# Kernel tuning notes

Measured on AMD Instinct MI355X. Metric: run time of the kernel, lower is better.

## Reference

```python
import jax, jax.numpy as jnp
import numpy as np

NH = 8       # num attention heads (hardcoded in module)
NL = 6       # n_layers
EPS = 1e-5   # LayerNorm eps (torch default)


def pos_enc(dim, length):
    # faithful to module's positional_encoding: even cols sin, odd cols cos,
    # with angle = pos / 10000^(2i/dim) where i indexes ALL columns via arange(0,2*dim,2)/dim
    pos = jnp.arange(length, dtype=jnp.float32)[:, None]
    div = 1.0 / (10000.0 ** (jnp.arange(0, 2 * dim, 2, dtype=jnp.float32) / dim))
    ang = pos * div[None, :]  # [length, dim]
    cols = jnp.arange(dim)
    return jnp.where(cols % 2 == 0, jnp.sin(ang), jnp.cos(ang))


def layernorm(x):
    m = x.mean(-1, keepdims=True)
    v = x.var(-1, keepdims=True)  # biased, matches torch LayerNorm
    return (x - m) / jnp.sqrt(v + EPS)


def setup_inputs() -> dict:
    key = jax.random.key(0)
    ks = jax.random.split(key, 8)
    S, H = 2048, 1024
    D = H // NH
    sc = 1.0 / np.sqrt(H)  # ~ torch Linear init scale
    return {
        "inputs": jax.random.normal(ks[0], (S, H), jnp.float32),
        "Wq": jax.random.normal(ks[1], (NH, H, D), jnp.float32) * sc,
        "bq": jnp.zeros((NH, D), jnp.float32),
        "Wk": jax.random.normal(ks[2], (NH, H, D), jnp.float32) * sc,
        "bk": jnp.zeros((NH, D), jnp.float32),
        "Wv": jax.random.normal(ks[3], (NH, H, D), jnp.float32) * sc,
        "bv": jnp.zeros((NH, D), jnp.float32),
        "W1": jax.random.normal(ks[4], (H, H), jnp.float32) * sc,
        "b1": jnp.zeros((H,), jnp.float32),
        "W2": jax.random.normal(ks[5], (H, H), jnp.float32) * sc,
        "b2": jnp.zeros((H,), jnp.float32),
    }


def reference(inputs, Wq, bq, Wk, bk, Wv, bv, W1, b1, W2, b2):
    S, H = inputs.shape
    scale = jnp.sqrt(jnp.float32(H))  # module scales by sqrt(hidden), not sqrt(head_dim)
    x = inputs + pos_enc(H, S)        # [S, H]
    kv = x  # dropout in eval mode = identity; k_v_input fixed to layer-0 input (faithful)
    # K/V are identical every layer (shared weights + fixed kv input)
    K = jnp.einsum('sh,nhd->nsd', kv, Wk) + bk[:, None, :]  # [NH, S, D]
    V = jnp.einsum('sh,nhd->nsd', kv, Wv) + bv[:, None, :]
    t_in = x
    for _ in range(NL):
        Q = jnp.einsum('sh,nhd->nsd', t_in, Wq) + bq[:, None, :]
        A = jax.nn.softmax(jnp.einsum('nsd,ntd->nst', Q, K) / scale, axis=-1)
        ctx = jnp.einsum('nst,ntd->nsd', A, V)        # [NH, S, D]
        cat = ctx.transpose(1, 0, 2).reshape(S, H)    # concat heads on feature dim
        mh = layernorm(t_in + cat)
        ff = jax.nn.relu(mh @ W1 + b1) @ W2 + b2
        t_in = layernorm(mh + ff)
    return t_in
```

## Files before the change

kernel.cpp:

```cpp
#include <hip/hip_runtime.h>

#define S_LEN 2048
#define H_DIM 1024
#define NHEAD 8
#define D_HEAD 128
#define KSPLIT 4
#define KV_PER (S_LEN / KSPLIT)

typedef __bf16 bf16x8 __attribute__((ext_vector_type(8)));
typedef float floatx4 __attribute__((ext_vector_type(4)));

__device__ __forceinline__ float b2f(unsigned short u) {
    union { unsigned int i; float f; } v;
    v.i = ((unsigned int)u) << 16;
    return v.f;
}
__device__ __forceinline__ unsigned short f2b(float f) {
    union { float f; unsigned int i; } v;
    v.f = f;
    return (unsigned short)((v.i + 0x7fffu + ((v.i >> 16) & 1u)) >> 16);
}

__device__ __forceinline__ void dma16(void* lds, const void* g) {
    __builtin_amdgcn_global_load_lds(
        (const __attribute__((address_space(1))) void*)g,
        (__attribute__((address_space(3))) void*)lds, 16, 0, 0);
}

__global__ __launch_bounds__(256) void posenc_kernel(
    const float* __restrict__ in, float* __restrict__ xf,
    unsigned short* __restrict__ xb)
{
    int g = blockIdx.x * 256 + threadIdx.x;
    int s = g >> 10;
    int h = g & 1023;
    float dv = powf(10000.0f, -(float)h * (1.0f / 512.0f));
    float ang = (float)s * dv;
    float pe = (h & 1) ? cosf(ang) : sinf(ang);
    float x = in[g] + pe;
    xf[g] = x;
    xb[g] = f2b(x);
}

__global__ __launch_bounds__(256) void transpose_f2b(
    const float* __restrict__ in, unsigned short* __restrict__ out, int R, int C)
{
    __shared__ unsigned short tile[32][33];
    const float* ih = in + (size_t)blockIdx.z * R * C;
    unsigned short* oh = out + (size_t)blockIdx.z * R * C;
    int r0 = blockIdx.y * 32, c0 = blockIdx.x * 32;
    int tx = threadIdx.x, ty = threadIdx.y;
    for (int i = ty; i < 32; i += 8)
        tile[i][tx] = f2b(ih[(size_t)(r0 + i) * C + c0 + tx]);
    __syncthreads();
    for (int i = ty; i < 32; i += 8)
        oh[(size_t)(c0 + i) * R + r0 + tx] = tile[tx][i];
}

template <int MODE, bool RELU>
__global__ __launch_bounds__(256, 4) void gemm_bt(
    const unsigned short* __restrict__ A, const unsigned short* __restrict__ Bt,
    const float* __restrict__ bias, float* __restrict__ Cf,
    unsigned short* __restrict__ Cb, int M, int N, int K, int ldt)
{
    __shared__ __align__(16) unsigned short sA[2][64 * 64];
    __shared__ __align__(16) unsigned short sB[2][64 * 64];
    const int tid = threadIdx.x;
    const int wave = tid >> 6, lane = tid & 63;
    const int quad = lane >> 4, l16 = lane & 15;
    const int i0 = blockIdx.y * 64, j0 = blockIdx.x * 64;
    const int wm = (wave >> 1) * 32, wn = (wave & 1) * 32;

    const int srow = lane >> 3;
    const int schunk = (lane & 7) ^ (srow & 7);
    const unsigned short* Ap0 = A + (size_t)(i0 + wave * 8 + srow) * K + schunk * 8;
    const unsigned short* Ap1 = A + (size_t)(i0 + 32 + wave * 8 + srow) * K + schunk * 8;
    const unsigned short* Bp0 = Bt + (size_t)(j0 + wave * 8 + srow) * K + schunk * 8;
    const unsigned short* Bp1 = Bt + (size_t)(j0 + 32 + wave * 8 + srow) * K + schunk * 8;
    const int ld0 = (wave * 8) * 64, ld1 = (32 + wave * 8) * 64;

    floatx4 z4 = {0.f, 0.f, 0.f, 0.f};
    floatx4 acc[2][2];
#pragma unroll
    for (int i = 0; i < 2; i++)
#pragma unroll
        for (int j = 0; j < 2; j++) acc[i][j] = z4;

    dma16(sA[0] + ld0, Ap0);
    dma16(sA[0] + ld1, Ap1);
    dma16(sB[0] + ld0, Bp0);
    dma16(sB[0] + ld1, Bp1);
    __syncthreads();

    int buf = 0;
    for (int k0 = 0; k0 < K; k0 += 64) {
        if (k0 + 64 < K) {
            dma16(sA[buf ^ 1] + ld0, Ap0 + k0 + 64);
            dma16(sA[buf ^ 1] + ld1, Ap1 + k0 + 64);
            dma16(sB[buf ^ 1] + ld0, Bp0 + k0 + 64);
            dma16(sB[buf ^ 1] + ld1, Bp1 + k0 + 64);
        }
        const unsigned short* cA = sA[buf];
        const unsigned short* cB = sB[buf];
#pragma unroll
        for (int kh = 0; kh < 2; kh++) {
            bf16x8 af[2], bfr[2];
#pragma unroll
            for (int mi = 0; mi < 2; mi++) {
                int row = wm + mi * 16 + l16;
                int p = (kh * 4 + quad) ^ (l16 & 7);
                af[mi] = *(const bf16x8*)(cA + row * 64 + p * 8);
            }
#pragma unroll
            for (int ni = 0; ni < 2; ni++) {
                int row = wn + ni * 16 + l16;
                int p = (kh * 4 + quad) ^ (l16 & 7);
                bfr[ni] = *(const bf16x8*)(cB + row * 64 + p * 8);
            }
#pragma unroll
            for (int mi = 0; mi < 2; mi++)
#pragma unroll
                for (int ni = 0; ni < 2; ni++)
                    acc[mi][ni] = __builtin_amdgcn_mfma_f32_16x16x32_bf16(
                        af[mi], bfr[ni], acc[mi][ni], 0, 0, 0);
        }
        __syncthreads();
        buf ^= 1;
    }

#pragma unroll
    for (int mi = 0; mi < 2; mi++) {
#pragma unroll
        for (int ni = 0; ni < 2; ni++) {
            const int col = j0 + wn + ni * 16 + l16;
            const float bval = bias[col];
#pragma unroll
            for (int r = 0; r < 4; r++) {
                const int row_o = i0 + wm + mi * 16 + quad * 4 + r;
                float v = acc[mi][ni][r] + bval;
                if (RELU) v = fmaxf(v, 0.0f);
                if (MODE == 0) Cb[(size_t)row_o * N + col] = f2b(v);
                else if (MODE == 1) Cb[(size_t)col * ldt + row_o] = f2b(v);
                else Cf[(size_t)row_o * N + col] = v;
            }
        }
    }
}

__global__ __launch_bounds__(256, 3) void flash_attn(
    const unsigned short* __restrict__ Qg, const unsigned short* __restrict__ Kg,
    const unsigned short* __restrict__ Vt, unsigned short* __restrict__ Op,
    float* __restrict__ Lp)
{
    __shared__ __align__(16) unsigned short sK[64 * 128];
    __shared__ __align__(16) unsigned short sV[128 * 64];

    const int tid = threadIdx.x;
    const int wave = tid >> 6, lane = tid & 63;
    const int quad = lane >> 4, l16 = lane & 15;
    const int head = blockIdx.y;
    const int q0 = blockIdx.x * 64;
    const int split = blockIdx.z;
    const int h0 = head * D_HEAD;

    bf16x8 aq[4];
    const int qrow = q0 + wave * 16 + l16;
#pragma unroll
    for (int ks = 0; ks < 4; ks++)
        aq[ks] = *(const bf16x8*)(Qg + (size_t)qrow * H_DIM + h0 + ks * 32 + quad * 8);

    unsigned short* myP = sK + wave * (16 * 72);

    const int k_r = wave * 4 + (lane >> 4);
    const int k_c = (lane & 15) ^ (k_r & 15);
    const int v_r = wave * 8 + (lane >> 3);
    const int v_c = (lane & 7) ^ (v_r & 7);

    const unsigned short* Kbase = Kg + h0;
    const unsigned short* Vbase = Vt + (size_t)h0 * S_LEN;
    const int kt0 = split * KV_PER;

    floatx4 z4 = {0.f, 0.f, 0.f, 0.f};
    floatx4 o[8];
#pragma unroll
    for (int i = 0; i < 8; i++) o[i] = z4;
    float l_r[4] = {0.f, 0.f, 0.f, 0.f};

    for (int it0 = 0; it0 < KV_PER; it0 += 64) {
        const int t0 = kt0 + it0;
        __syncthreads();
#pragma unroll
        for (int it = 0; it < 4; it++) {
            dma16(sK + (wave * 4 + it * 16) * 128,
                  Kbase + (size_t)(t0 + k_r + it * 16) * H_DIM + k_c * 8);
            dma16(sV + (wave * 8 + it * 32) * 64,
                  Vbase + (size_t)(v_r + it * 32) * S_LEN + t0 + v_c * 8);
        }
        __syncthreads();

        floatx4 sc[4];
#pragma unroll
        for (int ni = 0; ni < 4; ni++) {
            sc[ni] = z4;
#pragma unroll
            for (int ks = 0; ks < 4; ks++) {
                int p = (ks * 4 + quad) ^ l16;
                bf16x8 bk = *(const bf16x8*)(sK + (ni * 16 + l16) * 128 + p * 8);
                sc[ni] = __builtin_amdgcn_mfma_f32_16x16x32_bf16(aq[ks], bk, sc[ni], 0, 0, 0);
            }
        }

#pragma unroll
        for (int ni = 0; ni < 4; ni++)
#pragma unroll
            for (int r = 0; r < 4; r++) {
                float p = __expf(sc[ni][r] * 0.03125f);
                sc[ni][r] = p;
                l_r[r] += p;
            }

        __syncthreads();
#pragma unroll
        for (int ni = 0; ni < 4; ni++)
#pragma unroll
            for (int r = 0; r < 4; r++) {
                int prow = quad * 4 + r;
                myP[prow * 72 + ((ni * 16 + l16) ^ ((prow & 8) << 1))] = f2b(sc[ni][r]);
            }
        bf16x8 ap[2];
#pragma unroll
        for (int ks = 0; ks < 2; ks++)
            ap[ks] = *(const bf16x8*)(myP + l16 * 72 + ((ks * 32 + quad * 8) ^ ((l16 & 8) << 1)));
#pragma unroll
        for (int ni = 0; ni < 8; ni++) {
#pragma unroll
            for (int ks = 0; ks < 2; ks++) {
                int p = (ks * 4 + quad) ^ (l16 & 7);
                bf16x8 bv = *(const bf16x8*)(sV + (ni * 16 + l16) * 64 + p * 8);
                o[ni] = __builtin_amdgcn_mfma_f32_16x16x32_bf16(ap[ks], bv, o[ni], 0, 0, 0);
            }
        }
    }

#pragma unroll
    for (int r = 0; r < 4; r++)
#pragma unroll
        for (int off = 1; off < 16; off <<= 1)
            l_r[r] += __shfl_xor(l_r[r], off, 64);

#pragma unroll
    for (int r = 0; r < 4; r++) {
        float inv = 1.0f / l_r[r];
        int row = q0 + wave * 16 + quad * 4 + r;
#pragma unroll
        for (int ni = 0; ni < 8; ni++)
            Op[((size_t)split * S_LEN + row) * H_DIM + h0 + ni * 16 + l16] =
                f2b(o[ni][r] * inv);
        if (l16 == 0)
            Lp[(split * NHEAD + head) * S_LEN + row] = l_r[r];
    }
}

__global__ __launch_bounds__(256) void merge_add_layernorm(
    const float* __restrict__ t, const unsigned short* __restrict__ Op,
    const float* __restrict__ Lp,
    float* __restrict__ of, unsigned short* __restrict__ ob)
{
    __shared__ float red[8];
    const int row = blockIdx.x, tid = threadIdx.x;
    const int head = tid >> 5;
    const size_t base = (size_t)row * H_DIM + tid * 4;

    float l_s[KSPLIT];
    ushort4 os[KSPLIT];
#pragma unroll
    for (int sp = 0; sp < KSPLIT; sp++) {
        os[sp] = *(const ushort4*)(Op + ((size_t)sp * S_LEN + row) * H_DIM + tid * 4);
        l_s[sp] = Lp[(sp * NHEAD + head) * S_LEN + row];
    }
    float W = 0.f, a0 = 0.f, a1 = 0.f, a2 = 0.f, a3 = 0.f;
#pragma unroll
    for (int sp = 0; sp < KSPLIT; sp++) {
        float w = l_s[sp];
        W += w;
        a0 += w * b2f(os[sp].x);
        a1 += w * b2f(os[sp].y);
        a2 += w * b2f(os[sp].z);
        a3 += w * b2f(os[sp].w);
    }
    float inv = 1.0f / W;
    float4 x = *(const float4*)(t + base);
    float v0 = x.x + a0 * inv, v1 = x.y + a1 * inv;
    float v2 = x.z + a2 * inv, v3 = x.w + a3 * inv;

    float s = v0 + v1 + v2 + v3;
    float q = v0 * v0 + v1 * v1 + v2 * v2 + v3 * v3;
#pragma unroll
    for (int off = 32; off >= 1; off >>= 1) {
        s += __shfl_xor(s, off, 64);
        q += __shfl_xor(q, off, 64);
    }
    if ((tid & 63) == 0) { red[tid >> 6] = s; red[4 + (tid >> 6)] = q; }
    __syncthreads();
    s = red[0] + red[1] + red[2] + red[3];
    q = red[4] + red[5] + red[6] + red[7];
    const float mean = s * (1.0f / (float)H_DIM);
    const float var = q * (1.0f / (float)H_DIM) - mean * mean;
    const float rstd = rsqrtf(var + 1e-5f);
    float o0 = (v0 - mean) * rstd, o1 = (v1 - mean) * rstd;
    float o2 = (v2 - mean) * rstd, o3 = (v3 - mean) * rstd;
    *(float4*)(of + base) = make_float4(o0, o1, o2, o3);
    *(ushort4*)(ob + base) = make_ushort4(f2b(o0), f2b(o1), f2b(o2), f2b(o3));
}

__global__ __launch_bounds__(256) void add_layernorm(
    const float* __restrict__ a, const float* __restrict__ b,
    float* __restrict__ of, unsigned short* __restrict__ ob)
{
    __shared__ float red[8];
    const int row = blockIdx.x, tid = threadIdx.x;
    const size_t base = (size_t)row * H_DIM + tid * 4;
    float4 x = *(const float4*)(a + base);
    float4 y = *(const float4*)(b + base);
    float v0 = x.x + y.x, v1 = x.y + y.y, v2 = x.z + y.z, v3 = x.w + y.w;
    float s = v0 + v1 + v2 + v3;
    float q = v0 * v0 + v1 * v1 + v2 * v2 + v3 * v3;
#pragma unroll
    for (int off = 32; off >= 1; off >>= 1) {
        s += __shfl_xor(s, off, 64);
        q += __shfl_xor(q, off, 64);
    }
    if ((tid & 63) == 0) { red[tid >> 6] = s; red[4 + (tid >> 6)] = q; }
    __syncthreads();
    s = red[0] + red[1] + red[2] + red[3];
    q = red[4] + red[5] + red[6] + red[7];
    const float mean = s * (1.0f / (float)H_DIM);
    const float var = q * (1.0f / (float)H_DIM) - mean * mean;
    const float rstd = rsqrtf(var + 1e-5f);
    float o0 = (v0 - mean) * rstd, o1 = (v1 - mean) * rstd;
    float o2 = (v2 - mean) * rstd, o3 = (v3 - mean) * rstd;
    *(float4*)(of + base) = make_float4(o0, o1, o2, o3);
    *(ushort4*)(ob + base) = make_ushort4(f2b(o0), f2b(o1), f2b(o2), f2b(o3));
}

extern "C" void kernel_launch(void* const* d_in, const int* in_sizes, int n_in,
                              void* d_out, int out_size, void* d_ws, size_t ws_size,
                              hipStream_t stream)
{
    (void)in_sizes; (void)n_in; (void)out_size; (void)ws_size;
    const float* in = (const float*)d_in[0];
    const float* Wq = (const float*)d_in[1];
    const float* bq = (const float*)d_in[2];
    const float* Wk = (const float*)d_in[3];
    const float* bk = (const float*)d_in[4];
    const float* Wv = (const float*)d_in[5];
    const float* bv = (const float*)d_in[6];
    const float* W1 = (const float*)d_in[7];
    const float* b1 = (const float*)d_in[8];
    const float* W2 = (const float*)d_in[9];
    const float* b2 = (const float*)d_in[10];

    char* ws = (char*)d_ws;
    const size_t MB = 1024 * 1024;
    float* t_f32 = (float*)(ws + 0 * MB);
    float* cf_f32 = (float*)(ws + 8 * MB);
    unsigned short* t_b = (unsigned short*)(ws + 16 * MB);
    unsigned short* K_b = (unsigned short*)(ws + 20 * MB);
    unsigned short* Vt_b = (unsigned short*)(ws + 24 * MB);
    unsigned short* Q_b = (unsigned short*)(ws + 28 * MB);
    unsigned short* WqT = (unsigned short*)(ws + 32 * MB);
    unsigned short* WkT = (unsigned short*)(ws + 34 * MB);
    unsigned short* WvT = (unsigned short*)(ws + 36 * MB);
    unsigned short* W1T = (unsigned short*)(ws + 38 * MB);
    unsigned short* W2T = (unsigned short*)(ws + 40 * MB);
    unsigned short* Op = (unsigned short*)(ws + 42 * MB);
    float* Lp = (float*)(ws + 58 * MB);

    dim3 tb(32, 8);
    transpose_f2b<<<dim3(4, 32, 8), tb, 0, stream>>>(Wq, WqT, H_DIM, D_HEAD);
    transpose_f2b<<<dim3(4, 32, 8), tb, 0, stream>>>(Wk, WkT, H_DIM, D_HEAD);
    transpose_f2b<<<dim3(4, 32, 8), tb, 0, stream>>>(Wv, WvT, H_DIM, D_HEAD);
    transpose_f2b<<<dim3(32, 32, 1), tb, 0, stream>>>(W1, W1T, H_DIM, H_DIM);
    transpose_f2b<<<dim3(32, 32, 1), tb, 0, stream>>>(W2, W2T, H_DIM, H_DIM);

    posenc_kernel<<<(S_LEN * H_DIM) / 256, 256, 0, stream>>>(in, t_f32, t_b);

    dim3 gg(H_DIM / 64, S_LEN / 64);
    gemm_bt<0, false><<<gg, 256, 0, stream>>>(t_b, WkT, bk, nullptr, K_b, S_LEN, H_DIM, H_DIM, 0);
    gemm_bt<1, false><<<gg, 256, 0, stream>>>(t_b, WvT, bv, nullptr, Vt_b, S_LEN, H_DIM, H_DIM, S_LEN);

    for (int layer = 0; layer < 6; layer++) {
        gemm_bt<0, false><<<gg, 256, 0, stream>>>(t_b, WqT, bq, nullptr, Q_b, S_LEN, H_DIM, H_DIM, 0);
        flash_attn<<<dim3(S_LEN / 64, NHEAD, KSPLIT), 256, 0, stream>>>(Q_b, K_b, Vt_b, Op, Lp);
        merge_add_layernorm<<<S_LEN, 256, 0, stream>>>(t_f32, Op, Lp, t_f32, t_b);
        gemm_bt<0, true><<<gg, 256, 0, stream>>>(t_b, W1T, b1, nullptr, Q_b, S_LEN, H_DIM, H_DIM, 0);
        gemm_bt<2, false><<<gg, 256, 0, stream>>>(Q_b, W2T, b2, cf_f32, nullptr, S_LEN, H_DIM, H_DIM, 0);
        float* of = (layer == 5) ? (float*)d_out : t_f32;
        add_layernorm<<<S_LEN, 256, 0, stream>>>(t_f32, cf_f32, of, t_b);
    }
}
```

Before: 633.0 us.

## Double-buffer K/V tiles in flash attention and merge setup kernel launches

Flash attention now prefetches the next K/V tile into a second LDS buffer while computing on the current one, with a separate P scratch region. This removes one barrier per iteration and overlaps global loads with MFMA work. The five weight transposes are merged into one launch, and the K and V projections are merged into one GEMM launch. The extra LDS (about 73KB dynamic) lowers flash attention occupancy to 2 blocks per CU.

```diff
diff --git a/kernel.cpp b/kernel.cpp
--- a/kernel.cpp
+++ b/kernel.cpp
@@ -42,33 +42,43 @@
     xb[g] = f2b(x);
 }
 
-__global__ __launch_bounds__(256) void transpose_f2b(
-    const float* __restrict__ in, unsigned short* __restrict__ out, int R, int C)
+__global__ __launch_bounds__(256) void transpose_all(
+    const float* __restrict__ Wq, const float* __restrict__ Wk,
+    const float* __restrict__ Wv, const float* __restrict__ W1,
+    const float* __restrict__ W2,
+    unsigned short* __restrict__ WqT, unsigned short* __restrict__ WkT,
+    unsigned short* __restrict__ WvT, unsigned short* __restrict__ W1T,
+    unsigned short* __restrict__ W2T)
 {
     __shared__ unsigned short tile[32][33];
-    const float* ih = in + (size_t)blockIdx.z * R * C;
-    unsigned short* oh = out + (size_t)blockIdx.z * R * C;
-    int r0 = blockIdx.y * 32, c0 = blockIdx.x * 32;
-    int tx = threadIdx.x, ty = threadIdx.y;
+    const int z = blockIdx.z;
+    const float* ih;
+    unsigned short* oh;
+    int ldin;
+    if (z < 8)       { ih = Wq + (size_t)z * 131072;        oh = WqT + (size_t)z * 131072;        ldin = 128; }
+    else if (z < 16) { ih = Wk + (size_t)(z - 8) * 131072;  oh = WkT + (size_t)(z - 8) * 131072;  ldin = 128; }
+    else if (z < 24) { ih = Wv + (size_t)(z - 16) * 131072; oh = WvT + (size_t)(z - 16) * 131072; ldin = 128; }
+    else if (z < 32) { ih = W1 + (size_t)(z - 24) * 128;    oh = W1T + (size_t)(z - 24) * 131072; ldin = 1024; }
+    else             { ih = W2 + (size_t)(z - 32) * 128;    oh = W2T + (size_t)(z - 32) * 131072; ldin = 1024; }
+    const int r0 = blockIdx.y * 32, c0 = blockIdx.x * 32;
+    const int tx = threadIdx.x, ty = threadIdx.y;
     for (int i = ty; i < 32; i += 8)
-        tile[i][tx] = f2b(ih[(size_t)(r0 + i) * C + c0 + tx]);
+        tile[i][tx] = f2b(ih[(size_t)(r0 + i) * ldin + c0 + tx]);
     __syncthreads();
     for (int i = ty; i < 32; i += 8)
-        oh[(size_t)(c0 + i) * R + r0 + tx] = tile[tx][i];
+        oh[(size_t)(c0 + i) * 1024 + r0 + tx] = tile[tx][i];
 }
 
 template <int MODE, bool RELU>
-__global__ __launch_bounds__(256, 4) void gemm_bt(
-    const unsigned short* __restrict__ A, const unsigned short* __restrict__ Bt,
-    const float* __restrict__ bias, float* __restrict__ Cf,
-    unsigned short* __restrict__ Cb, int M, int N, int K, int ldt)
-{
-    __shared__ __align__(16) unsigned short sA[2][64 * 64];
-    __shared__ __align__(16) unsigned short sB[2][64 * 64];
+__device__ __forceinline__ void gemm_core(
+    unsigned short* sA0, unsigned short* sB0,
+    const unsigned short* A, const unsigned short* Bt,
+    const float* bias, float* Cf, unsigned short* Cb,
+    int N, int K, int ldt, int i0, int j0)
+{
     const int tid = threadIdx.x;
     const int wave = tid >> 6, lane = tid & 63;
     const int quad = lane >> 4, l16 = lane & 15;
-    const int i0 = blockIdx.y * 64, j0 = blockIdx.x * 64;
     const int wm = (wave >> 1) * 32, wn = (wave & 1) * 32;
 
     const int srow = lane >> 3;
@@ -86,22 +96,24 @@
 #pragma unroll
         for (int j = 0; j < 2; j++) acc[i][j] = z4;
 
-    dma16(sA[0] + ld0, Ap0);
-    dma16(sA[0] + ld1, Ap1);
-    dma16(sB[0] + ld0, Bp0);
-    dma16(sB[0] + ld1, Bp1);
+    dma16(sA0 + ld0, Ap0);
+    dma16(sA0 + ld1, Ap1);
+    dma16(sB0 + ld0, Bp0);
+    dma16(sB0 + ld1, Bp1);
     __syncthreads();
 
     int buf = 0;
     for (int k0 = 0; k0 < K; k0 += 64) {
         if (k0 + 64 < K) {
-            dma16(sA[buf ^ 1] + ld0, Ap0 + k0 + 64);
-            dma16(sA[buf ^ 1] + ld1, Ap1 + k0 + 64);
-            dma16(sB[buf ^ 1] + ld0, Bp0 + k0 + 64);
-            dma16(sB[buf ^ 1] + ld1, Bp1 + k0 + 64);
-        }
-        const unsigned short* cA = sA[buf];
-        const unsigned short* cB = sB[buf];
+            unsigned short* nA = sA0 + (buf ^ 1) * 4096;
+            unsigned short* nB = sB0 + (buf ^ 1) * 4096;
+            dma16(nA + ld0, Ap0 + k0 + 64);
+            dma16(nA + ld1, Ap1 + k0 + 64);
+            dma16(nB + ld0, Bp0 + k0 + 64);
+            dma16(nB + ld1, Bp1 + k0 + 64);
+        }
+        const unsigned short* cA = sA0 + buf * 4096;
+        const unsigned short* cB = sB0 + buf * 4096;
 #pragma unroll
         for (int kh = 0; kh < 2; kh++) {
             bf16x8 af[2], bfr[2];
@@ -147,13 +159,43 @@
     }
 }
 
-__global__ __launch_bounds__(256, 3) void flash_attn(
+template <int MODE, bool RELU>
+__global__ __launch_bounds__(256, 4) void gemm_bt(
+    const unsigned short* __restrict__ A, const unsigned short* __restrict__ Bt,
+    const float* __restrict__ bias, float* __restrict__ Cf,
+    unsigned short* __restrict__ Cb, int M, int N, int K, int ldt)
+{
+    __shared__ __align__(16) unsigned short sA[2 * 64 * 64];
+    __shared__ __align__(16) unsigned short sB[2 * 64 * 64];
+    gemm_core<MODE, RELU>(sA, sB, A, Bt, bias, Cf, Cb, N, K, ldt,
+                          blockIdx.y * 64, blockIdx.x * 64);
+}
+
+__global__ __launch_bounds__(256, 4) void gemm_kv(
+    const unsigned short* __restrict__ A,
+    const unsigned short* __restrict__ WkT, const unsigned short* __restrict__ WvT,
+    const float* __restrict__ bk, const float* __restrict__ bv,
+    unsigned short* __restrict__ Kb, unsigned short* __restrict__ Vtb)
+{
+    __shared__ __align__(16) unsigned short sA[2 * 64 * 64];
+    __shared__ __align__(16) unsigned short sB[2 * 64 * 64];
+    if (blockIdx.z == 0)
+        gemm_core<0, false>(sA, sB, A, WkT, bk, nullptr, Kb, H_DIM, H_DIM, 0,
+                            blockIdx.y * 64, blockIdx.x * 64);
+    else
+        gemm_core<1, false>(sA, sB, A, WvT, bv, nullptr, Vtb, H_DIM, H_DIM, S_LEN,
+                            blockIdx.y * 64, blockIdx.x * 64);
+}
+
+__global__ __launch_bounds__(256, 2) void flash_attn(
     const unsigned short* __restrict__ Qg, const unsigned short* __restrict__ Kg,
     const unsigned short* __restrict__ Vt, unsigned short* __restrict__ Op,
     float* __restrict__ Lp)
 {
-    __shared__ __align__(16) unsigned short sK[64 * 128];
-    __shared__ __align__(16) unsigned short sV[128 * 64];
+    extern __shared__ __align__(16) unsigned short smem[];
+    unsigned short* sK0 = smem;
+    unsigned short* sV0 = smem + 16384;
+    unsigned short* sP = smem + 32768;
 
     const int tid = threadIdx.x;
     const int wave = tid >> 6, lane = tid & 63;
@@ -169,7 +211,7 @@
     for (int ks = 0; ks < 4; ks++)
         aq[ks] = *(const bf16x8*)(Qg + (size_t)qrow * H_DIM + h0 + ks * 32 + quad * 8);
 
-    unsigned short* myP = sK + wave * (16 * 72);
+    unsigned short* myP = sP + wave * (16 * 72);
 
     const int k_r = wave * 4 + (lane >> 4);
     const int k_c = (lane & 15) ^ (k_r & 15);
@@ -186,17 +228,32 @@
     for (int i = 0; i < 8; i++) o[i] = z4;
     float l_r[4] = {0.f, 0.f, 0.f, 0.f};
 
+#pragma unroll
+    for (int it = 0; it < 4; it++) {
+        dma16(sK0 + (wave * 4 + it * 16) * 128,
+              Kbase + (size_t)(kt0 + k_r + it * 16) * H_DIM + k_c * 8);
+        dma16(sV0 + (wave * 8 + it * 32) * 64,
+              Vbase + (size_t)(v_r + it * 32) * S_LEN + kt0 + v_c * 8);
+    }
+    __syncthreads();
+
+    int buf = 0;
     for (int it0 = 0; it0 < KV_PER; it0 += 64) {
         const int t0 = kt0 + it0;
-        __syncthreads();
-#pragma unroll
-        for (int it = 0; it < 4; it++) {
-            dma16(sK + (wave * 4 + it * 16) * 128,
-                  Kbase + (size_t)(t0 + k_r + it * 16) * H_DIM + k_c * 8);
-            dma16(sV + (wave * 8 + it * 32) * 64,
-                  Vbase + (size_t)(v_r + it * 32) * S_LEN + t0 + v_c * 8);
-        }
-        __syncthreads();
+        if (it0 + 64 < KV_PER) {
+            const int nt = t0 + 64;
+            unsigned short* nK = sK0 + (buf ^ 1) * 8192;
+            unsigned short* nV = sV0 + (buf ^ 1) * 8192;
+#pragma unroll
+            for (int it = 0; it < 4; it++) {
+                dma16(nK + (wave * 4 + it * 16) * 128,
+                      Kbase + (size_t)(nt + k_r + it * 16) * H_DIM + k_c * 8);
+                dma16(nV + (wave * 8 + it * 32) * 64,
+                      Vbase + (size_t)(v_r + it * 32) * S_LEN + nt + v_c * 8);
+            }
+        }
+        const unsigned short* cK = sK0 + buf * 8192;
+        const unsigned short* cV = sV0 + buf * 8192;
 
         floatx4 sc[4];
 #pragma unroll
@@ -205,7 +262,7 @@
 #pragma unroll
             for (int ks = 0; ks < 4; ks++) {
                 int p = (ks * 4 + quad) ^ l16;
-                bf16x8 bk = *(const bf16x8*)(sK + (ni * 16 + l16) * 128 + p * 8);
+                bf16x8 bk = *(const bf16x8*)(cK + (ni * 16 + l16) * 128 + p * 8);
                 sc[ni] = __builtin_amdgcn_mfma_f32_16x16x32_bf16(aq[ks], bk, sc[ni], 0, 0, 0);
             }
         }
@@ -219,7 +276,6 @@
                 l_r[r] += p;
             }
 
-        __syncthreads();
 #pragma unroll
         for (int ni = 0; ni < 4; ni++)
 #pragma unroll
@@ -231,15 +287,19 @@
 #pragma unroll
         for (int ks = 0; ks < 2; ks++)
             ap[ks] = *(const bf16x8*)(myP + l16 * 72 + ((ks * 32 + quad * 8) ^ ((l16 & 8) << 1)));
+
 #pragma unroll
         for (int ni = 0; ni < 8; ni++) {
 #pragma unroll
             for (int ks = 0; ks < 2; ks++) {
                 int p = (ks * 4 + quad) ^ (l16 & 7);
-                bf16x8 bv = *(const bf16x8*)(sV + (ni * 16 + l16) * 64 + p * 8);
+                bf16x8 bv = *(const bf16x8*)(cV + (ni * 16 + l16) * 64 + p * 8);
                 o[ni] = __builtin_amdgcn_mfma_f32_16x16x32_bf16(ap[ks], bv, o[ni], 0, 0, 0);
             }
         }
+
+        __syncthreads();
+        buf ^= 1;
     }
 
 #pragma unroll
@@ -376,22 +436,20 @@
     unsigned short* Op = (unsigned short*)(ws + 42 * MB);
     float* Lp = (float*)(ws + 58 * MB);
 
-    dim3 tb(32, 8);
-    transpose_f2b<<<dim3(4, 32, 8), tb, 0, stream>>>(Wq, WqT, H_DIM, D_HEAD);
-    transpose_f2b<<<dim3(4, 32, 8), tb, 0, stream>>>(Wk, WkT, H_DIM, D_HEAD);
-    transpose_f2b<<<dim3(4, 32, 8), tb, 0, stream>>>(Wv, WvT, H_DIM, D_HEAD);
-    transpose_f2b<<<dim3(32, 32, 1), tb, 0, stream>>>(W1, W1T, H_DIM, H_DIM);
-    transpose_f2b<<<dim3(32, 32, 1), tb, 0, stream>>>(W2, W2T, H_DIM, H_DIM);
+    (void)hipFuncSetAttribute(reinterpret_cast<const void*>(&flash_attn),
+                              hipFuncAttributeMaxDynamicSharedMemorySize, 74752);
+
+    transpose_all<<<dim3(4, 32, 40), dim3(32, 8), 0, stream>>>(
+        Wq, Wk, Wv, W1, W2, WqT, WkT, WvT, W1T, W2T);
 
     posenc_kernel<<<(S_LEN * H_DIM) / 256, 256, 0, stream>>>(in, t_f32, t_b);
 
     dim3 gg(H_DIM / 64, S_LEN / 64);
-    gemm_bt<0, false><<<gg, 256, 0, stream>>>(t_b, WkT, bk, nullptr, K_b, S_LEN, H_DIM, H_DIM, 0);
-    gemm_bt<1, false><<<gg, 256, 0, stream>>>(t_b, WvT, bv, nullptr, Vt_b, S_LEN, H_DIM, H_DIM, S_LEN);
+    gemm_kv<<<dim3(16, 32, 2), 256, 0, stream>>>(t_b, WkT, WvT, bk, bv, K_b, Vt_b);
 
     for (int layer = 0; layer < 6; layer++) {
         gemm_bt<0, false><<<gg, 256, 0, stream>>>(t_b, WqT, bq, nullptr, Q_b, S_LEN, H_DIM, H_DIM, 0);
-        flash_attn<<<dim3(S_LEN / 64, NHEAD, KSPLIT), 256, 0, stream>>>(Q_b, K_b, Vt_b, Op, Lp);
+        flash_attn<<<dim3(S_LEN / 64, NHEAD, KSPLIT), 256, 74752, stream>>>(Q_b, K_b, Vt_b, Op, Lp);
         merge_add_layernorm<<<S_LEN, 256, 0, stream>>>(t_f32, Op, Lp, t_f32, t_b);
         gemm_bt<0, true><<<gg, 256, 0, stream>>>(t_b, W1T, b1, nullptr, Q_b, S_LEN, H_DIM, H_DIM, 0);
         gemm_bt<2, false><<<gg, 256, 0, stream>>>(Q_b, W2T, b2, cf_f32, nullptr, S_LEN, H_DIM, H_DIM, 0);
```

After: 598.0 us. 5.5% less time.
